# Performance work log

Measured on AMD Instinct MI355X. Metric: run time of the kernel, lower is better.

Reference implementation:

```python
import jax, jax.numpy as jnp
import numpy as np

B = 64
N_TOTAL = 131072
C_ENC = 128   # base_channels * 4
CTX = 128     # context_dim
HID = 512     # hidden_dim
YDIM = 3
TDIM = 64
HEADS = 4


def timestep_embedding(t, dim=TDIM):
    half = dim // 2
    freqs = jnp.exp(-jnp.arange(half, dtype=jnp.float32) * (np.log(10000.0) / half))
    args = t[:, None].astype(jnp.float32) * freqs[None, :]
    return jnp.concatenate([jnp.sin(args), jnp.cos(args)], axis=-1)


def setup_inputs() -> dict:
    key = jax.random.key(0)
    ks = jax.random.split(key, 32)
    s = 0.05
    p = lambda k, shape: (jax.random.normal(k, shape, jnp.float32) * s)
    inp = {
        "features": jax.random.normal(ks[0], (N_TOTAL, C_ENC), jnp.float32),
        "batch_idx": jnp.sort(jax.random.randint(ks[1], (N_TOTAL,), 0, B)),
        "y_t": jax.random.normal(ks[2], (B, YDIM), jnp.float32),
        "t": jax.random.randint(ks[3], (B,), 0, 1000),
        "N_max": 3328,
        # token_pool
        "Wtok": p(ks[4], (C_ENC, CTX)), "btok": jnp.zeros((CTX,)),
        # time_mlp
        "Wt": p(ks[5], (TDIM, HID)), "bt": jnp.zeros((HID,)),
        # input_proj
        "Win": p(ks[6], (YDIM, HID)), "bin_": jnp.zeros((HID,)),
        # cross-attn pre-projections
        "Wq": p(ks[7], (HID, CTX)), "bq": jnp.zeros((CTX,)),
        "Wk": p(ks[8], (CTX, CTX)), "bk": jnp.zeros((CTX,)),
        "Wv": p(ks[9], (CTX, CTX)), "bv": jnp.zeros((CTX,)),
        # nn.MultiheadAttention in_proj (q,k,v) and out_proj
        "Wiq": p(ks[10], (CTX, CTX)), "biq": jnp.zeros((CTX,)),
        "Wik": p(ks[11], (CTX, CTX)), "bik": jnp.zeros((CTX,)),
        "Wiv": p(ks[12], (CTX, CTX)), "biv": jnp.zeros((CTX,)),
        "Wo": p(ks[13], (CTX, CTX)), "bo": jnp.zeros((CTX,)),
        # cross-attn out: context_dim -> hidden_dim
        "Wco": p(ks[14], (CTX, HID)), "bco": jnp.zeros((HID,)),
        # final output: hidden -> y_dim
        "Wout": p(ks[15], (HID, YDIM)), "bout": jnp.zeros((YDIM,)),
    }
    return inp


def reference(features, batch_idx, y_t, t, N_max,
              Wtok, btok, Wt, bt, Win, bin_, Wq, bq, Wk, bk, Wv, bv,
              Wiq, biq, Wik, bik, Wiv, biv, Wo, bo, Wco, bco, Wout, bout):
    Bsz = y_t.shape[0]
    N = features.shape[0]
    dh = CTX // HEADS

    # encoder token_pool
    feat = features @ Wtok + btok                                      # [N, CTX]

    # fused to_dense_batch: scatter by (batch, within-batch position)
    counts = jax.ops.segment_sum(jnp.ones((N,), jnp.int32), batch_idx,
                                 num_segments=Bsz)                      # [B]
    starts = jnp.cumsum(counts) - counts                                # exclusive cumsum
    pos = jnp.arange(N, dtype=jnp.int32) - starts[batch_idx]            # [N]
    context = jnp.zeros((Bsz, N_max, CTX), feat.dtype).at[batch_idx, pos].set(feat)
    pad_mask = jnp.arange(N_max)[None, :] >= counts[:, None]            # True = padding

    # diffusion head
    t_h = jax.nn.relu(timestep_embedding(t) @ Wt + bt)                  # [B, HID]
    y = y_t @ Win + bin_ + t_h                                          # [B, HID]

    # cross-attention: query=y (1 token), keys/values=context tokens
    q0 = (y @ Wq + bq)                                                  # [B, CTX]
    k0 = context @ Wk + bk                                              # [B, Nm, CTX]
    v0 = context @ Wv + bv
    # MultiheadAttention internal projections
    q = (q0 @ Wiq + biq).reshape(Bsz, HEADS, dh)                        # [B, H, dh]
    k = (k0 @ Wik + bik).reshape(Bsz, N_max, HEADS, dh)
    v = (v0 @ Wiv + biv).reshape(Bsz, N_max, HEADS, dh)
    scores = jnp.einsum('bhd,bnhd->bhn', q, k) / np.sqrt(dh)            # [B, H, Nm]
    scores = jnp.where(pad_mask[:, None, :], -1e9, scores)
    attn = jax.nn.softmax(scores, axis=-1)
    ctx_out = jnp.einsum('bhn,bnhd->bhd', attn, v).reshape(Bsz, CTX)
    attn_out = ctx_out @ Wo + bo                                        # [B, CTX]

    y2 = attn_out @ Wco + bco                                           # [B, HID]
    return y2 @ Wout + bout                                             # [B, YDIM]
```

## Files before the change

### kernel.cpp

```cpp
#include <hip/hip_runtime.h>
#include <hip/hip_bf16.h>


typedef unsigned short ushort_t;
typedef unsigned int uint_t;
typedef unsigned long long ull_t;

#define NB 64
#define CENC 128
#define HID 512
#define RSQRT32 0.17677669529663689f

#define WS_FLAG   0
#define WS_CNT    64
#define WS_SLOT   128
#define WS_U      2176
#define WS_CQ     34944
#define WS_LOVF   35200
#define WS_WOVF   35456
#define WS_LPART  68224
#define WS_WPART  76416

__device__ __forceinline__ float bf2f(ushort_t h){ return __uint_as_float(((uint_t)h) << 16); }
__device__ __forceinline__ ushort_t f2bf(float f){
    uint_t u = __float_as_uint(f);
    u += 0x7fffu + ((u >> 16) & 1u);
    return (ushort_t)(u >> 16);
}

template<bool BF16> struct Ld;
template<> struct Ld<true> {
    static __device__ __forceinline__ float at(const void* p, long i) {
        return __uint_as_float(((uint_t)((const ushort_t*)p)[i]) << 16);
    }
};
template<> struct Ld<false> {
    static __device__ __forceinline__ float at(const void* p, long i) {
        return ((const float*)p)[i];
    }
};

__device__ int detect_bf16(const ushort_t* f, int tid, int* sh2) {
    if (tid == 0) { sh2[0] = 0; sh2[1] = 0; }
    __syncthreads();
    int myb = 0, myz = 0;
    for (int i = tid; i < 4096; i += 256) {
        ushort_t v = f[i];
        if (((v >> 7) & 0xff) >= 140) myb = 1;
        if (!(i & 1) && v == 0) myz++;
    }
    if (myb) atomicOr(&sh2[0], 1);
    atomicAdd(&sh2[1], myz);
    __syncthreads();
    return (sh2[0] || sh2[1] > 1024) ? 0 : 1;
}

template<bool BF16>
__device__ void kA_impl(int b, int tid,
    const void* y_t, const int* t,
    const void* Wt, const void* bt, const void* Win, const void* bin_,
    const void* Wq, const void* bq, const void* Wiq, const void* biq,
    const void* Wtok, const void* btok, const void* Wk, const void* bk,
    const void* Wik, const void* bik, float* ws, float* sh)
{
    using L = Ld<BF16>;
    float* emb = sh;
    float* y   = sh + 64;
    float* p2  = sh + 576;
    float* q0  = sh + 832;
    float* qL  = sh + 960;
    float* tb  = sh + 1088;
    float* t1a = sh + 1216;
    float* t2a = sh + 1728;
    float* p1k = sh + 2240;
    float* u_out  = ws + WS_U;
    float* cq_out = ws + WS_CQ;

    const int c = tid & 127, pair = tid >> 7;

    for (int i = tid; i < 512; i += 256) ws[WS_WOVF + b*512 + i] = 0.f;
    if (tid < 4) ws[WS_LOVF + b*4 + tid] = 0.f;
    if (tid == 0) ((int*)ws)[WS_CNT + b] = 0;

    if (tid < 32) {
        float fr = __expf(-(float)tid * 0.28782313662425576f);
        float arg = (float)t[b] * fr;
        emb[tid]      = sinf(arg);
        emb[tid + 32] = cosf(arg);
    }
    __syncthreads();

    float yt0 = L::at(y_t, b*3+0), yt1 = L::at(y_t, b*3+1), yt2 = L::at(y_t, b*3+2);
    #pragma unroll
    for (int rep = 0; rep < 2; rep++) {
        int o = tid + rep*256;
        float acc = L::at(bt, o);
        #pragma unroll
        for (int k = 0; k < 64; k++) acc += emb[k] * L::at(Wt, (long)k*512 + o);
        acc = fmaxf(acc, 0.f);
        y[o] = acc + L::at(bin_, o) + yt0*L::at(Win, o) + yt1*L::at(Win, 512+o)
             + yt2*L::at(Win, 1024+o);
    }
    __syncthreads();
    {
        float acc = 0.f;
        #pragma unroll
        for (int k4 = 0; k4 < 256; k4 += 4) {
            int kk = pair*256 + k4;
            float4 y4 = *(const float4*)&y[kk];
            acc += y4.x*L::at(Wq,(long)kk*128+c)     + y4.y*L::at(Wq,(long)(kk+1)*128+c)
                 + y4.z*L::at(Wq,(long)(kk+2)*128+c) + y4.w*L::at(Wq,(long)(kk+3)*128+c);
        }
        p2[pair*128 + c] = acc;
    }
    __syncthreads();
    if (tid < 128) q0[tid] = p2[tid] + p2[128+tid] + L::at(bq, tid);
    __syncthreads();
    {
        float acc = 0.f;
        #pragma unroll
        for (int k4 = 0; k4 < 64; k4 += 4) {
            int kk = pair*64 + k4;
            float4 q4 = *(const float4*)&q0[kk];
            acc += q4.x*L::at(Wiq,(long)kk*128+c)     + q4.y*L::at(Wiq,(long)(kk+1)*128+c)
                 + q4.z*L::at(Wiq,(long)(kk+2)*128+c) + q4.w*L::at(Wiq,(long)(kk+3)*128+c);
        }
        p2[pair*128 + c] = acc;
    }
    __syncthreads();
    if (tid < 128) qL[tid] = p2[tid] + p2[128+tid] + L::at(biq, tid);
    __syncthreads();
    {
        float acc = 0.f;
        #pragma unroll
        for (int k4 = 0; k4 < 64; k4 += 4) {
            int kk = pair*64 + k4;
            acc += L::at(btok,kk)  *L::at(Wk,(long)kk*128+c)
                 + L::at(btok,kk+1)*L::at(Wk,(long)(kk+1)*128+c)
                 + L::at(btok,kk+2)*L::at(Wk,(long)(kk+2)*128+c)
                 + L::at(btok,kk+3)*L::at(Wk,(long)(kk+3)*128+c);
        }
        p2[pair*128 + c] = acc;
    }
    __syncthreads();
    if (tid < 128) tb[tid] = p2[tid] + p2[128+tid] + L::at(bk, tid);
    __syncthreads();
    {
        float a0=0.f, a1=0.f, a2=0.f, a3=0.f;
        #pragma unroll
        for (int j = 0; j < 16; j++) {
            int jj = pair*16 + j;
            a0 += L::at(Wik,(long)c*128 +  0 + jj) * qL[ 0 + jj];
            a1 += L::at(Wik,(long)c*128 + 32 + jj) * qL[32 + jj];
            a2 += L::at(Wik,(long)c*128 + 64 + jj) * qL[64 + jj];
            a3 += L::at(Wik,(long)c*128 + 96 + jj) * qL[96 + jj];
        }
        p1k[pair*512 +   0 + c] = a0; p1k[pair*512 + 128 + c] = a1;
        p1k[pair*512 + 256 + c] = a2; p1k[pair*512 + 384 + c] = a3;
    }
    __syncthreads();
    t1a[tid]     = p1k[tid]     + p1k[512+tid];
    t1a[tid+256] = p1k[tid+256] + p1k[768+tid];
    __syncthreads();
    {
        int hw = tid >> 6, lam = tid & 63;
        float r = tb[lam]*t1a[hw*128+lam] + tb[lam+64]*t1a[hw*128+64+lam];
        if (lam < 32) r += L::at(bik, hw*32+lam) * qL[hw*32+lam];
        #pragma unroll
        for (int mm = 1; mm < 64; mm <<= 1) r += __shfl_xor(r, mm, 64);
        if (lam == 0) cq_out[b*4 + hw] = r * RSQRT32;
    }
    {
        float a0=0.f, a1=0.f, a2=0.f, a3=0.f;
        #pragma unroll
        for (int k4 = 0; k4 < 64; k4 += 4) {
            int kk = pair*64 + k4;
            float wa = L::at(Wk,(long)c*128+kk),   wbv = L::at(Wk,(long)c*128+kk+1);
            float wc = L::at(Wk,(long)c*128+kk+2), wd  = L::at(Wk,(long)c*128+kk+3);
            float4 t0 = *(const float4*)&t1a[kk],     t1v = *(const float4*)&t1a[128+kk];
            float4 t2v = *(const float4*)&t1a[256+kk], t3v = *(const float4*)&t1a[384+kk];
            a0 += wa*t0.x + wbv*t0.y + wc*t0.z + wd*t0.w;
            a1 += wa*t1v.x + wbv*t1v.y + wc*t1v.z + wd*t1v.w;
            a2 += wa*t2v.x + wbv*t2v.y + wc*t2v.z + wd*t2v.w;
            a3 += wa*t3v.x + wbv*t3v.y + wc*t3v.z + wd*t3v.w;
        }
        p1k[pair*512 +   0 + c] = a0; p1k[pair*512 + 128 + c] = a1;
        p1k[pair*512 + 256 + c] = a2; p1k[pair*512 + 384 + c] = a3;
    }
    __syncthreads();
    t2a[tid]     = p1k[tid]     + p1k[512+tid];
    t2a[tid+256] = p1k[tid+256] + p1k[768+tid];
    __syncthreads();
    {
        float a0=0.f, a1=0.f, a2=0.f, a3=0.f;
        #pragma unroll
        for (int k4 = 0; k4 < 64; k4 += 4) {
            int kk = pair*64 + k4;
            float wa = L::at(Wtok,(long)c*128+kk),   wbv = L::at(Wtok,(long)c*128+kk+1);
            float wc = L::at(Wtok,(long)c*128+kk+2), wd  = L::at(Wtok,(long)c*128+kk+3);
            float4 t0 = *(const float4*)&t2a[kk],     t1v = *(const float4*)&t2a[128+kk];
            float4 t2v = *(const float4*)&t2a[256+kk], t3v = *(const float4*)&t2a[384+kk];
            a0 += wa*t0.x + wbv*t0.y + wc*t0.z + wd*t0.w;
            a1 += wa*t1v.x + wbv*t1v.y + wc*t1v.z + wd*t1v.w;
            a2 += wa*t2v.x + wbv*t2v.y + wc*t2v.z + wd*t2v.w;
            a3 += wa*t3v.x + wbv*t3v.y + wc*t3v.z + wd*t3v.w;
        }
        p1k[pair*512 +   0 + c] = a0; p1k[pair*512 + 128 + c] = a1;
        p1k[pair*512 + 256 + c] = a2; p1k[pair*512 + 384 + c] = a3;
    }
    __syncthreads();
    u_out[b*512 + tid]     = (p1k[tid]     + p1k[512+tid]) * RSQRT32;
    u_out[b*512 + tid+256] = (p1k[tid+256] + p1k[768+tid]) * RSQRT32;
}

__global__ __launch_bounds__(256) void kA(
    const ushort_t* __restrict__ fraw,
    const void* y_t, const int* t,
    const void* Wt, const void* bt, const void* Win, const void* bin_,
    const void* Wq, const void* bq, const void* Wiq, const void* biq,
    const void* Wtok, const void* btok, const void* Wk, const void* bk,
    const void* Wik, const void* bik, float* ws)
{
    __shared__ int sh2[2];
    __shared__ float sh[3264];
    int flag = detect_bf16(fraw, threadIdx.x, sh2);
    if (blockIdx.x == 0 && threadIdx.x == 0) *(int*)(ws + WS_FLAG) = flag;
    if (flag) kA_impl<true >(blockIdx.x, threadIdx.x, y_t,t,Wt,bt,Win,bin_,Wq,bq,
                             Wiq,biq,Wtok,btok,Wk,bk,Wik,bik, ws, sh);
    else      kA_impl<false>(blockIdx.x, threadIdx.x, y_t,t,Wt,bt,Win,bin_,Wq,bq,
                             Wiq,biq,Wtok,btok,Wk,bk,Wik,bik, ws, sh);
}

template<bool BF16>
__device__ void kF_impl(const void* F, const int* __restrict__ batch_idx,
                        float* __restrict__ ws, int blk)
{
    using L = Ld<BF16>;
    __shared__ float eL[512];
    __shared__ float pp[2048];
    __shared__ float red[8];
    __shared__ int lb[128];
    __shared__ int starts[129];
    __shared__ ull_t smask[2];
    __shared__ int nsegs;
    __shared__ int segslot[2];

    const int base = blk * 128;
    const int tau = threadIdx.x;
    const float* u   = ws + WS_U;
    const float* cqg = ws + WS_CQ;
    int* cnt      = (int*)ws + WS_CNT;
    int* slotlist = (int*)ws + WS_SLOT;
    float* l_ovf  = ws + WS_LOVF;
    float* w_ovf  = ws + WS_WOVF;
    float* lpart  = ws + WS_LPART;
    ushort_t* wpart = (ushort_t*)(ws + WS_WPART);

    if (tau < 128) lb[tau] = batch_idx[base + tau];
    __syncthreads();
    bool isstart = (tau < 128) && (tau == 0 || lb[tau] != lb[tau-1]);
    ull_t m = __ballot(isstart);
    const int wv = tau >> 6, lane = tau & 63;
    if (wv < 2 && lane == 0) smask[wv] = m;
    __syncthreads();
    if (isstart) {
        int rank = ((wv == 1) ? __popcll(smask[0]) : 0)
                 + __popcll(m & ((1ull << lane) - 1ull));
        starts[rank] = tau;
    }
    if (tau == 0) nsegs = __popcll(smask[0]) + __popcll(smask[1]);
    __syncthreads();
    const int nseg = nsegs;
    if (tau < 2) {
        int ss = -1;
        if (tau < nseg) {
            int bb = lb[starts[tau]];
            int idx = atomicAdd(&cnt[bb], 1);
            if (idx < 32) { slotlist[bb*32 + idx] = blk*2 + tau; ss = blk*2 + tau; }
        }
        segslot[tau] = ss;
    }
    __syncthreads();

    const int tok = tau & 127;
    const int hp  = __builtin_amdgcn_readfirstlane(tau >> 7);
    const int cA  = tau & 63, cB = cA + 64, sg4 = tau >> 6;

    for (int s = 0; s < nseg; s++) {
        const int lo = starts[s];
        const int hi = (s + 1 < nseg) ? starts[s+1] : 128;
        const int b  = lb[lo];
        const int slot = (s < 2) ? segslot[s] : -1;

        const float* ur0 = u + b*512 + (2*hp)*128;
        const float* ur1 = ur0 + 128;
        float cq0 = cqg[b*4 + 2*hp], cq1 = cqg[b*4 + 2*hp + 1];
        bool act = (tok >= lo) && (tok < hi);
        float d0 = 0.f, d1 = 0.f;
        if (act) {
            long row = (long)(base + tok) * 128;
            #pragma unroll
            for (int k = 0; k < 128; k += 4) {
                float fa = L::at(F, row+k),   fb = L::at(F, row+k+1);
                float fc = L::at(F, row+k+2), fd = L::at(F, row+k+3);
                d0 += fa*ur0[k] + fb*ur0[k+1] + fc*ur0[k+2] + fd*ur0[k+3];
                d1 += fa*ur1[k] + fb*ur1[k+1] + fc*ur1[k+2] + fd*ur1[k+3];
            }
        }
        float e0 = act ? __expf(fminf(d0 + cq0, 30.f)) : 0.f;
        float e1 = act ? __expf(fminf(d1 + cq1, 30.f)) : 0.f;
        if (act) *(float2*)&eL[tok*4 + 2*hp] = make_float2(e0, e1);
        float s0 = e0, s1 = e1;
        #pragma unroll
        for (int mm = 1; mm < 64; mm <<= 1) {
            s0 += __shfl_xor(s0, mm, 64);
            s1 += __shfl_xor(s1, mm, 64);
        }
        if (lane == 0) { red[wv*2] = s0; red[wv*2+1] = s1; }
        __syncthreads();

        if (tau < 4) {
            int h = tau, g = h >> 1, j = h & 1;
            float ls = red[g*4 + j] + red[g*4 + 2 + j];
            if (slot >= 0) lpart[slot*4 + h] = ls;
            else atomicAdd(&l_ovf[b*4 + h], ls);
        }

        float a0=0.f,a1=0.f,a2=0.f,a3=0.f,a4=0.f,a5=0.f,a6=0.f,a7=0.f;
        int tk = lo + sg4;
        for (; tk + 4 < hi; tk += 8) {
            float4 e0v = *(const float4*)&eL[tk*4];
            float4 e1v = *(const float4*)&eL[(tk+4)*4];
            float fA0 = L::at(F, (long)(base+tk)*128 + cA);
            float fB0 = L::at(F, (long)(base+tk)*128 + cB);
            float fA1 = L::at(F, (long)(base+tk+4)*128 + cA);
            float fB1 = L::at(F, (long)(base+tk+4)*128 + cB);
            a0 += e0v.x*fA0 + e1v.x*fA1; a1 += e0v.y*fA0 + e1v.y*fA1;
            a2 += e0v.z*fA0 + e1v.z*fA1; a3 += e0v.w*fA0 + e1v.w*fA1;
            a4 += e0v.x*fB0 + e1v.x*fB1; a5 += e0v.y*fB0 + e1v.y*fB1;
            a6 += e0v.z*fB0 + e1v.z*fB1; a7 += e0v.w*fB0 + e1v.w*fB1;
        }
        for (; tk < hi; tk += 4) {
            float4 ev = *(const float4*)&eL[tk*4];
            float fA = L::at(F, (long)(base+tk)*128 + cA);
            float fB = L::at(F, (long)(base+tk)*128 + cB);
            a0 += ev.x*fA; a1 += ev.y*fA; a2 += ev.z*fA; a3 += ev.w*fA;
            a4 += ev.x*fB; a5 += ev.y*fB; a6 += ev.z*fB; a7 += ev.w*fB;
        }
        int col = sg4*64 + cA;
        pp[0*256+col]=a0; pp[1*256+col]=a1; pp[2*256+col]=a2; pp[3*256+col]=a3;
        pp[4*256+col]=a4; pp[5*256+col]=a5; pp[6*256+col]=a6; pp[7*256+col]=a7;
        __syncthreads();
        #pragma unroll
        for (int rep = 0; rep < 2; rep++) {
            int i = tau + rep*256;
            int h = i >> 7, ch = i & 127;
            int comp = (ch < 64) ? h : (h + 4);
            int cc = ch & 63;
            float v = pp[comp*256 +   0 + cc] + pp[comp*256 +  64 + cc]
                    + pp[comp*256 + 128 + cc] + pp[comp*256 + 192 + cc];
            if (slot >= 0) wpart[(long)slot*512 + i] = f2bf(v);
            else atomicAdd(&w_ovf[b*512 + i], v);
        }
        __syncthreads();
    }
}

__global__ __launch_bounds__(256) void kF(
    const void* __restrict__ features, const int* __restrict__ batch_idx,
    float* __restrict__ ws)
{
    if (*(const int*)(ws + WS_FLAG)) kF_impl<true >(features, batch_idx, ws, blockIdx.x);
    else                             kF_impl<false>(features, batch_idx, ws, blockIdx.x);
}

template<bool BF16>
__device__ void kE_impl(int b, int tid, float* ws,
    const void* Wtok, const void* btok, const void* Wv, const void* bv,
    const void* Wiv, const void* biv, const void* Wo, const void* bo,
    const void* Wco, const void* bco, const void* Wout, const void* bout,
    void* out, float* sh, int* shi)
{
    using L = Ld<BF16>;
    float* wb   = sh;
    float* s1a  = sh + 512;
    float* s2a  = sh + 1024;
    float* ctxa = sh + 1536;
    float* aoa  = sh + 1664;
    float* y2a  = sh + 1792;
    float* p1k  = sh + 2304;
    float* linv = sh + 3328;

    const int c = tid & 127, pair = tid >> 7;
    const int* cnti = (const int*)ws;
    const ushort_t* wpart = (const ushort_t*)(ws + WS_WPART);

    int n = cnti[WS_CNT + b]; if (n > 32) n = 32;
    if (tid < 32) shi[tid] = (tid < n) ? cnti[WS_SLOT + b*32 + tid] : 0;
    __syncthreads();

    float a0 = 0.f, a1 = 0.f, lac = 0.f;
    for (int i = 0; i < n; i++) {
        int s = shi[i];
        a0 += bf2f(wpart[(long)s*512 + tid]);
        a1 += bf2f(wpart[(long)s*512 + tid + 256]);
    }
    if (tid < 4) for (int i = 0; i < n; i++) lac += ws[WS_LPART + shi[i]*4 + tid];
    a0 += ws[WS_WOVF + b*512 + tid];
    a1 += ws[WS_WOVF + b*512 + tid + 256];
    if (tid < 4) {
        lac += ws[WS_LOVF + b*4 + tid];
        linv[tid] = (lac > 1e-30f) ? 1.f/lac : 0.f;
    }
    __syncthreads();
    wb[tid]     = a0 * linv[tid >> 7];
    wb[tid+256] = a1 * linv[(tid+256) >> 7];
    __syncthreads();

    {
        float b0=0.f,b1=0.f,b2=0.f,b3=0.f;
        #pragma unroll
        for (int k4 = 0; k4 < 64; k4 += 4) {
            int kk = pair*64 + k4;
            float wa = L::at(Wtok,(long)kk*128+c),     wbv = L::at(Wtok,(long)(kk+1)*128+c);
            float wc = L::at(Wtok,(long)(kk+2)*128+c), wd  = L::at(Wtok,(long)(kk+3)*128+c);
            float4 w0 = *(const float4*)&wb[kk],     w1 = *(const float4*)&wb[128+kk];
            float4 w2 = *(const float4*)&wb[256+kk], w3 = *(const float4*)&wb[384+kk];
            b0 += wa*w0.x + wbv*w0.y + wc*w0.z + wd*w0.w;
            b1 += wa*w1.x + wbv*w1.y + wc*w1.z + wd*w1.w;
            b2 += wa*w2.x + wbv*w2.y + wc*w2.z + wd*w2.w;
            b3 += wa*w3.x + wbv*w3.y + wc*w3.z + wd*w3.w;
        }
        p1k[pair*512 +   0 + c] = b0; p1k[pair*512 + 128 + c] = b1;
        p1k[pair*512 + 256 + c] = b2; p1k[pair*512 + 384 + c] = b3;
    }
    __syncthreads();
    s1a[tid]     = p1k[tid]     + p1k[512+tid]     + L::at(btok, tid & 127);
    s1a[tid+256] = p1k[tid+256] + p1k[768+tid]     + L::at(btok, (tid+256) & 127);
    __syncthreads();
    {
        float b0=0.f,b1=0.f,b2=0.f,b3=0.f;
        #pragma unroll
        for (int k4 = 0; k4 < 64; k4 += 4) {
            int kk = pair*64 + k4;
            float wa = L::at(Wv,(long)kk*128+c),     wbv = L::at(Wv,(long)(kk+1)*128+c);
            float wc = L::at(Wv,(long)(kk+2)*128+c), wd  = L::at(Wv,(long)(kk+3)*128+c);
            float4 w0 = *(const float4*)&s1a[kk],     w1 = *(const float4*)&s1a[128+kk];
            float4 w2 = *(const float4*)&s1a[256+kk], w3 = *(const float4*)&s1a[384+kk];
            b0 += wa*w0.x + wbv*w0.y + wc*w0.z + wd*w0.w;
            b1 += wa*w1.x + wbv*w1.y + wc*w1.z + wd*w1.w;
            b2 += wa*w2.x + wbv*w2.y + wc*w2.z + wd*w2.w;
            b3 += wa*w3.x + wbv*w3.y + wc*w3.z + wd*w3.w;
        }
        p1k[pair*512 +   0 + c] = b0; p1k[pair*512 + 128 + c] = b1;
        p1k[pair*512 + 256 + c] = b2; p1k[pair*512 + 384 + c] = b3;
    }
    __syncthreads();
    s2a[tid]     = p1k[tid]     + p1k[512+tid] + L::at(bv, tid & 127);
    s2a[tid+256] = p1k[tid+256] + p1k[768+tid] + L::at(bv, (tid+256) & 127);
    __syncthreads();
    {
        int h = c >> 5;
        float acc = 0.f;
        #pragma unroll
        for (int k4 = 0; k4 < 64; k4 += 4) {
            int kk = pair*64 + k4;
            float4 s4 = *(const float4*)&s2a[h*128 + kk];
            acc += s4.x*L::at(Wiv,(long)kk*128+c)     + s4.y*L::at(Wiv,(long)(kk+1)*128+c)
                 + s4.z*L::at(Wiv,(long)(kk+2)*128+c) + s4.w*L::at(Wiv,(long)(kk+3)*128+c);
        }
        p1k[pair*128 + c] = acc;
    }
    __syncthreads();
    if (tid < 128) ctxa[tid] = p1k[tid] + p1k[128+tid] + L::at(biv, tid);
    __syncthreads();
    {
        float acc = 0.f;
        #pragma unroll
        for (int k4 = 0; k4 < 64; k4 += 4) {
            int kk = pair*64 + k4;
            float4 c4 = *(const float4*)&ctxa[kk];
            acc += c4.x*L::at(Wo,(long)kk*128+c)     + c4.y*L::at(Wo,(long)(kk+1)*128+c)
                 + c4.z*L::at(Wo,(long)(kk+2)*128+c) + c4.w*L::at(Wo,(long)(kk+3)*128+c);
        }
        p1k[pair*128 + c] = acc;
    }
    __syncthreads();
    if (tid < 128) aoa[tid] = p1k[tid] + p1k[128+tid] + L::at(bo, tid);
    __syncthreads();
    {
        float acc0 = 0.f, acc1 = 0.f;
        #pragma unroll
        for (int k = 0; k < 128; k += 4) {
            float4 a4 = *(const float4*)&aoa[k];
            acc0 += a4.x*L::at(Wco,(long)k*512+tid)     + a4.y*L::at(Wco,(long)(k+1)*512+tid)
                  + a4.z*L::at(Wco,(long)(k+2)*512+tid) + a4.w*L::at(Wco,(long)(k+3)*512+tid);
            acc1 += a4.x*L::at(Wco,(long)k*512+tid+256)     + a4.y*L::at(Wco,(long)(k+1)*512+tid+256)
                  + a4.z*L::at(Wco,(long)(k+2)*512+tid+256) + a4.w*L::at(Wco,(long)(k+3)*512+tid+256);
        }
        y2a[tid]     = acc0 + L::at(bco, tid);
        y2a[tid+256] = acc1 + L::at(bco, tid+256);
    }
    __syncthreads();
    for (int o = 0; o < 3; o++) {
        float p = y2a[tid]*L::at(Wout,(long)tid*3+o)
                + y2a[tid+256]*L::at(Wout,(long)(tid+256)*3+o);
        p1k[tid] = p; __syncthreads();
        for (int st = 128; st > 0; st >>= 1) {
            if (tid < st) p1k[tid] += p1k[tid+st];
            __syncthreads();
        }
        if (tid == 0) {
            float val = p1k[0] + L::at(bout, o);
            if (BF16) ((ushort_t*)out)[b*3+o] = f2bf(val);
            else      ((float*)out)[b*3+o] = val;
        }
        __syncthreads();
    }
}

__global__ __launch_bounds__(256) void kE(
    float* ws,
    const void* Wtok, const void* btok, const void* Wv, const void* bv,
    const void* Wiv, const void* biv, const void* Wo, const void* bo,
    const void* Wco, const void* bco, const void* Wout, const void* bout,
    void* out)
{
    __shared__ float sh[3332];
    __shared__ int shi[32];
    if (*(const int*)(ws + WS_FLAG))
        kE_impl<true >(blockIdx.x, threadIdx.x, ws, Wtok,btok,Wv,bv,Wiv,biv,
                       Wo,bo,Wco,bco,Wout,bout,out,sh,shi);
    else
        kE_impl<false>(blockIdx.x, threadIdx.x, ws, Wtok,btok,Wv,bv,Wiv,biv,
                       Wo,bo,Wco,bco,Wout,bout,out,sh,shi);
}

extern "C" void kernel_launch(void* const* d_in, const int* in_sizes, int n_in,
                              void* d_out, int out_size, void* d_ws, size_t ws_size,
                              hipStream_t stream)
{
    const void* features = d_in[0];
    const int*  batch_idx= (const int*)d_in[1];
    const void* y_t      = d_in[2];
    const int*  t        = (const int*)d_in[3];
    const void *Wtok=d_in[5],  *btok=d_in[6];
    const void *Wt  =d_in[7],  *bt  =d_in[8];
    const void *Win =d_in[9],  *bin_=d_in[10];
    const void *Wq  =d_in[11], *bq  =d_in[12];
    const void *Wk  =d_in[13], *bk  =d_in[14];
    const void *Wv  =d_in[15], *bv  =d_in[16];
    const void *Wiq =d_in[17], *biq =d_in[18];
    const void *Wik =d_in[19], *bik =d_in[20];
    const void *Wiv =d_in[21], *biv =d_in[22];
    const void *Wo  =d_in[23], *bo  =d_in[24];
    const void *Wco =d_in[25], *bco =d_in[26];
    const void *Wout=d_in[27], *bout=d_in[28];

    int N = in_sizes[0] / CENC;
    float* ws = (float*)d_ws;

    kA<<<NB, 256, 0, stream>>>((const ushort_t*)features, y_t, t,
        Wt, bt, Win, bin_, Wq, bq, Wiq, biq, Wtok, btok, Wk, bk, Wik, bik, ws);
    kF<<<N / 128, 256, 0, stream>>>(features, batch_idx, ws);
    kE<<<NB, 256, 0, stream>>>(ws, Wtok, btok, Wv, bv, Wiv, biv, Wo, bo,
                               Wco, bco, Wout, bout, d_out);
}
```

Baseline: 217.8 us.

## Vectorize feature loads in kF with per-row 16-lane split and shuffle reduction

Restructures the kF score phase so 16 lanes share one token row, each loading 8 contiguous channels as one vector (uint4 for bf16, float4 for fp32), computing all four head dot products and reducing with 16-wide shuffles. The previous version had each thread walk a full row with scalar loads. The weighted-sum phase now has each thread load a channel pair per token, and the partial-sum buffer uses a padded layout so the final reduction is a simple strided add. Launch bounds now request 4 blocks per CU. The goal is coalesced, wider global loads and less redundant work, at the cost of extra shuffles and possible register pressure.

After: 201.6 us. -7.4%, faster.

```diff
diff --git a/kernel.cpp b/kernel.cpp
--- a/kernel.cpp
+++ b/kernel.cpp
@@ -21,6 +21,8 @@
 #define WS_LPART  68224
 #define WS_WPART  76416
 
+__device__ __forceinline__ float blo(uint_t u){ return __uint_as_float(u << 16); }
+__device__ __forceinline__ float bhi(uint_t u){ return __uint_as_float(u & 0xffff0000u); }
 __device__ __forceinline__ float bf2f(ushort_t h){ return __uint_as_float(((uint_t)h) << 16); }
 __device__ __forceinline__ ushort_t f2bf(float f){
     uint_t u = __float_as_uint(f);
@@ -231,14 +233,18 @@
                              Wiq,biq,Wtok,btok,Wk,bk,Wik,bik, ws, sh);
 }
 
+__device__ __forceinline__ float dot8(float4 fa, float4 fb, float4 ua, float4 ub) {
+    return fa.x*ua.x + fa.y*ua.y + fa.z*ua.z + fa.w*ua.w
+         + fb.x*ub.x + fb.y*ub.y + fb.z*ub.z + fb.w*ub.w;
+}
+
 template<bool BF16>
 __device__ void kF_impl(const void* F, const int* __restrict__ batch_idx,
                         float* __restrict__ ws, int blk)
 {
-    using L = Ld<BF16>;
     __shared__ float eL[512];
-    __shared__ float pp[2048];
-    __shared__ float red[8];
+    __shared__ float pp[4*520];
+    __shared__ float red[16];
     __shared__ int lb[128];
     __shared__ int starts[129];
     __shared__ ull_t smask[2];
@@ -282,9 +288,8 @@
     }
     __syncthreads();
 
-    const int tok = tau & 127;
-    const int hp  = __builtin_amdgcn_readfirstlane(tau >> 7);
-    const int cA  = tau & 63, cB = cA + 64, sg4 = tau >> 6;
+    const int qq = tau & 15, grp = tau >> 4;
+    const int cp = tau & 63, grp4 = tau >> 6;
 
     for (int s = 0; s < nseg; s++) {
         const int lo = starts[s];
@@ -292,73 +297,85 @@
         const int b  = lb[lo];
         const int slot = (s < 2) ? segslot[s] : -1;
 
-        const float* ur0 = u + b*512 + (2*hp)*128;
-        const float* ur1 = ur0 + 128;
-        float cq0 = cqg[b*4 + 2*hp], cq1 = cqg[b*4 + 2*hp + 1];
-        bool act = (tok >= lo) && (tok < hi);
-        float d0 = 0.f, d1 = 0.f;
-        if (act) {
-            long row = (long)(base + tok) * 128;
+        const float* ub = u + b*512 + qq*8;
+        float4 u0a = *(const float4*)(ub + 0),   u0b = *(const float4*)(ub + 4);
+        float4 u1a = *(const float4*)(ub + 128), u1b = *(const float4*)(ub + 132);
+        float4 u2a = *(const float4*)(ub + 256), u2b = *(const float4*)(ub + 260);
+        float4 u3a = *(const float4*)(ub + 384), u3b = *(const float4*)(ub + 388);
+        float4 cqr = *(const float4*)(cqg + b*4);
+
+        float l0=0.f, l1=0.f, l2=0.f, l3=0.f;
+        #pragma unroll 2
+        for (int tok = lo + grp; tok < hi; tok += 16) {
+            float4 fa, fb;
+            if (BF16) {
+                uint4 v = *(const uint4*)((const ushort_t*)F + ((long)(base+tok) << 7) + (qq << 3));
+                fa.x=blo(v.x); fa.y=bhi(v.x); fa.z=blo(v.y); fa.w=bhi(v.y);
+                fb.x=blo(v.z); fb.y=bhi(v.z); fb.z=blo(v.w); fb.w=bhi(v.w);
+            } else {
+                const float4* fp = (const float4*)((const float*)F + ((long)(base+tok) << 7) + (qq << 3));
+                fa = fp[0]; fb = fp[1];
+            }
+            float p0 = dot8(fa, fb, u0a, u0b);
+            float p1 = dot8(fa, fb, u1a, u1b);
+            float p2 = dot8(fa, fb, u2a, u2b);
+            float p3 = dot8(fa, fb, u3a, u3b);
             #pragma unroll
-            for (int k = 0; k < 128; k += 4) {
-                float fa = L::at(F, row+k),   fb = L::at(F, row+k+1);
-                float fc = L::at(F, row+k+2), fd = L::at(F, row+k+3);
-                d0 += fa*ur0[k] + fb*ur0[k+1] + fc*ur0[k+2] + fd*ur0[k+3];
-                d1 += fa*ur1[k] + fb*ur1[k+1] + fc*ur1[k+2] + fd*ur1[k+3];
+            for (int mm = 1; mm < 16; mm <<= 1) {
+                p0 += __shfl_xor(p0, mm, 16);
+                p1 += __shfl_xor(p1, mm, 16);
+                p2 += __shfl_xor(p2, mm, 16);
+                p3 += __shfl_xor(p3, mm, 16);
             }
-        }
-        float e0 = act ? __expf(fminf(d0 + cq0, 30.f)) : 0.f;
-        float e1 = act ? __expf(fminf(d1 + cq1, 30.f)) : 0.f;
-        if (act) *(float2*)&eL[tok*4 + 2*hp] = make_float2(e0, e1);
-        float s0 = e0, s1 = e1;
-        #pragma unroll
-        for (int mm = 1; mm < 64; mm <<= 1) {
-            s0 += __shfl_xor(s0, mm, 64);
-            s1 += __shfl_xor(s1, mm, 64);
-        }
-        if (lane == 0) { red[wv*2] = s0; red[wv*2+1] = s1; }
+            float e0 = __expf(fminf(p0 + cqr.x, 30.f));
+            float e1 = __expf(fminf(p1 + cqr.y, 30.f));
+            float e2 = __expf(fminf(p2 + cqr.z, 30.f));
+            float e3 = __expf(fminf(p3 + cqr.w, 30.f));
+            if (qq == 0) *(float4*)&eL[tok*4] = make_float4(e0, e1, e2, e3);
+            l0 += e0; l1 += e1; l2 += e2; l3 += e3;
+        }
+        l0 += __shfl_xor(l0, 16, 64); l1 += __shfl_xor(l1, 16, 64);
+        l2 += __shfl_xor(l2, 16, 64); l3 += __shfl_xor(l3, 16, 64);
+        l0 += __shfl_xor(l0, 32, 64); l1 += __shfl_xor(l1, 32, 64);
+        l2 += __shfl_xor(l2, 32, 64); l3 += __shfl_xor(l3, 32, 64);
+        if (lane == 0) *(float4*)&red[wv*4] = make_float4(l0, l1, l2, l3);
         __syncthreads();
 
         if (tau < 4) {
-            int h = tau, g = h >> 1, j = h & 1;
-            float ls = red[g*4 + j] + red[g*4 + 2 + j];
-            if (slot >= 0) lpart[slot*4 + h] = ls;
-            else atomicAdd(&l_ovf[b*4 + h], ls);
-        }
-
-        float a0=0.f,a1=0.f,a2=0.f,a3=0.f,a4=0.f,a5=0.f,a6=0.f,a7=0.f;
-        int tk = lo + sg4;
-        for (; tk + 4 < hi; tk += 8) {
-            float4 e0v = *(const float4*)&eL[tk*4];
-            float4 e1v = *(const float4*)&eL[(tk+4)*4];
-            float fA0 = L::at(F, (long)(base+tk)*128 + cA);
-            float fB0 = L::at(F, (long)(base+tk)*128 + cB);
-            float fA1 = L::at(F, (long)(base+tk+4)*128 + cA);
-            float fB1 = L::at(F, (long)(base+tk+4)*128 + cB);
-            a0 += e0v.x*fA0 + e1v.x*fA1; a1 += e0v.y*fA0 + e1v.y*fA1;
-            a2 += e0v.z*fA0 + e1v.z*fA1; a3 += e0v.w*fA0 + e1v.w*fA1;
-            a4 += e0v.x*fB0 + e1v.x*fB1; a5 += e0v.y*fB0 + e1v.y*fB1;
-            a6 += e0v.z*fB0 + e1v.z*fB1; a7 += e0v.w*fB0 + e1v.w*fB1;
-        }
-        for (; tk < hi; tk += 4) {
-            float4 ev = *(const float4*)&eL[tk*4];
-            float fA = L::at(F, (long)(base+tk)*128 + cA);
-            float fB = L::at(F, (long)(base+tk)*128 + cB);
-            a0 += ev.x*fA; a1 += ev.y*fA; a2 += ev.z*fA; a3 += ev.w*fA;
-            a4 += ev.x*fB; a5 += ev.y*fB; a6 += ev.z*fB; a7 += ev.w*fB;
-        }
-        int col = sg4*64 + cA;
-        pp[0*256+col]=a0; pp[1*256+col]=a1; pp[2*256+col]=a2; pp[3*256+col]=a3;
-        pp[4*256+col]=a4; pp[5*256+col]=a5; pp[6*256+col]=a6; pp[7*256+col]=a7;
+            float ls = red[tau] + red[4+tau] + red[8+tau] + red[12+tau];
+            if (slot >= 0) lpart[slot*4 + tau] = ls;
+            else atomicAdd(&l_ovf[b*4 + tau], ls);
+        }
+
+        float a00=0.f,a01=0.f,a10=0.f,a11=0.f,a20=0.f,a21=0.f,a30=0.f,a31=0.f;
+        #pragma unroll 2
+        for (int tk = lo + grp4; tk < hi; tk += 4) {
+            float f0, f1;
+            if (BF16) {
+                uint_t v = *(const uint_t*)((const ushort_t*)F + ((long)(base+tk) << 7) + (cp << 1));
+                f0 = blo(v); f1 = bhi(v);
+            } else {
+                float2 v = *(const float2*)((const float*)F + ((long)(base+tk) << 7) + (cp << 1));
+                f0 = v.x; f1 = v.y;
+            }
+            float4 e = *(const float4*)&eL[tk*4];
+            a00 += e.x*f0; a01 += e.x*f1;
+            a10 += e.y*f0; a11 += e.y*f1;
+            a20 += e.z*f0; a21 += e.z*f1;
+            a30 += e.w*f0; a31 += e.w*f1;
+        }
+        {
+            float* pr = pp + grp4*520;
+            *(float2*)&pr[  0 + 2*cp] = make_float2(a00, a01);
+            *(float2*)&pr[128 + 2*cp] = make_float2(a10, a11);
+            *(float2*)&pr[256 + 2*cp] = make_float2(a20, a21);
+            *(float2*)&pr[384 + 2*cp] = make_float2(a30, a31);
+        }
         __syncthreads();
         #pragma unroll
         for (int rep = 0; rep < 2; rep++) {
             int i = tau + rep*256;
-            int h = i >> 7, ch = i & 127;
-            int comp = (ch < 64) ? h : (h + 4);
-            int cc = ch & 63;
-            float v = pp[comp*256 +   0 + cc] + pp[comp*256 +  64 + cc]
-                    + pp[comp*256 + 128 + cc] + pp[comp*256 + 192 + cc];
+            float v = pp[i] + pp[520 + i] + pp[1040 + i] + pp[1560 + i];
             if (slot >= 0) wpart[(long)slot*512 + i] = f2bf(v);
             else atomicAdd(&w_ovf[b*512 + i], v);
         }
@@ -366,7 +383,7 @@
     }
 }
 
-__global__ __launch_bounds__(256) void kF(
+__global__ __launch_bounds__(256, 4) void kF(
     const void* __restrict__ features, const int* __restrict__ batch_idx,
     float* __restrict__ ws)
 {
```
